# Kernel optimization log

Measured on AMD Instinct MI355X. Metric: run time of the kernel, lower is better.

## Reference

```python
import jax, jax.numpy as jnp
import numpy as np

NUM_FREQ = 10
HIDDEN = 256
ENC_DIM = 2 * 2 * NUM_FREQ  # input_dim * 2 * num_frequencies = 40
OUT_DIM = 3


def setup_inputs() -> dict:
    key = jax.random.key(0)
    ks = jax.random.split(key, 8)
    B, N = 4, 262144
    x = jax.random.uniform(ks[0], (B, N, 2), dtype=jnp.float32)
    # layer 0: enc_dim -> hidden
    W_in = jax.random.normal(ks[1], (ENC_DIM, HIDDEN), dtype=jnp.float32) * (1.0 / np.sqrt(ENC_DIM))
    b_in = jnp.zeros((HIDDEN,), dtype=jnp.float32)
    # layers 1..6: hidden -> hidden (6 of them)
    W_hid = jax.random.normal(ks[2], (6, HIDDEN, HIDDEN), dtype=jnp.float32) * (1.0 / np.sqrt(HIDDEN))
    b_hid = jnp.zeros((6, HIDDEN), dtype=jnp.float32)
    # layer 7: hidden -> out
    W_out = jax.random.normal(ks[3], (HIDDEN, OUT_DIM), dtype=jnp.float32) * (1.0 / np.sqrt(HIDDEN))
    b_out = jnp.zeros((OUT_DIM,), dtype=jnp.float32)
    return {"x": x, "W_in": W_in, "b_in": b_in, "W_hid": W_hid,
            "b_hid": b_hid, "W_out": W_out, "b_out": b_out}


def _pos_encode(x):
    # x: (B, N, 2) -> (B, N, 40). Matches torch: cat([sin, cos], -1) over freq axis then flatten.
    freq = 2.0 ** jnp.arange(NUM_FREQ, dtype=jnp.float32)  # (10,)
    xe = x[..., :, None] * freq  # (B, N, 2, 10)
    enc = jnp.concatenate([jnp.sin(xe), jnp.cos(xe)], axis=-1)  # (B, N, 2, 20)
    return enc.reshape(x.shape[0], x.shape[1], -1)  # (B, N, 40)


def reference(x, W_in, b_in, W_hid, b_hid, W_out, b_out):
    h = _pos_encode(x)
    h = jax.nn.relu(h @ W_in + b_in)
    for i in range(W_hid.shape[0]):  # 6 hidden layers, fixed small loop
        h = jax.nn.relu(h @ W_hid[i] + b_hid[i])
    out = jnp.tanh(h @ W_out + b_out) / 100.0
    return out
```

## Files before the change

kernel.cpp:

```cpp
#include <hip/hip_runtime.h>
#include <stdint.h>

#define THREADS 512
#define NBLOCKS 8192
#define BR      128

#define NG_STRIDE 204800
#define WS_WOUT   819200
#define WS_TOTAL  (WS_WOUT + 16384)

typedef short bf16x8 __attribute__((ext_vector_type(8)));
typedef float f32x16 __attribute__((ext_vector_type(16)));
typedef float f32x4v __attribute__((ext_vector_type(4)));

__device__ __forceinline__ unsigned short f2bf(float f) {
    union { float f; unsigned int u; } v; v.f = f;
    unsigned int u = v.u;
    u += 0x7fffu + ((u >> 16) & 1u);
    return (unsigned short)(u >> 16);
}
__device__ __forceinline__ unsigned int cvt_pk_bf16(float lo, float hi) {
    unsigned int d;
    asm("v_cvt_pk_bf16_f32 %0, %1, %2" : "=v"(d) : "v"(lo), "v"(hi));
    return d;
}

__global__ void prep_kernel(const float* __restrict__ W_in,
                            const float* __restrict__ W_hid,
                            const float* __restrict__ W_out,
                            unsigned char* __restrict__ ws) {
    int id = blockIdx.x * 256 + threadIdx.x;
    if (id < 16384) {
        int n = id & 255, k = id >> 8;
        int ng = n >> 6, ft = (n >> 5) & 1, ln = n & 31;
        int kk = k >> 4, hi = (k >> 3) & 1, e = k & 7;
        float v = (k < 40) ? W_in[k * 256 + n] : 0.f;
        *(unsigned short*)(ws + ng * NG_STRIDE + (kk * 2 + ft) * 1024
                           + (hi * 32 + ln) * 16 + e * 2) = f2bf(v);
    } else if (id < 16384 + 393216) {
        int e2 = id - 16384;
        int l = e2 >> 16, r = e2 & 65535;
        int k = r >> 8, n = r & 255;
        int c = k >> 6, kk = (k >> 4) & 3, hi = (k >> 3) & 1, e = k & 7;
        int ng = n >> 6, ft = (n >> 5) & 1, ln = n & 31;
        float v = W_hid[l * 65536 + k * 256 + n];
        *(unsigned short*)(ws + ng * NG_STRIDE + 8192 + l * 32768
                           + ((c * 4 + kk) * 2 + ft) * 1024
                           + (hi * 32 + ln) * 16 + e * 2) = f2bf(v);
    } else if (id < 16384 + 393216 + 8192) {
        int e3 = id - 16384 - 393216;
        int n = e3 >> 8, k = e3 & 255;
        int kk = k >> 4, hi = (k >> 3) & 1, e = k & 7;
        float v = (n < 3) ? W_out[k * 3 + n] : 0.f;
        *(unsigned short*)(ws + WS_WOUT + kk * 1024
                           + (hi * 32 + n) * 16 + e * 2) = f2bf(v);
    }
}

template <int NC>
__device__ __forceinline__ void layer_pass(const unsigned char* __restrict__ wl,
                                           const float* __restrict__ bp,
                                           unsigned char* actL, f32x16 (&acc)[2][2],
                                           int nblk, int rblk, int l31,
                                           int hi, int hi16, int swz) {
    #pragma unroll
    for (int tn = 0; tn < 2; ++tn) {
        #pragma unroll
        for (int g4 = 0; g4 < 4; ++g4) {
            f32x4v bv = *(const f32x4v*)(bp + nblk + tn * 32 + g4 * 8 + hi * 4);
            #pragma unroll
            for (int j = 0; j < 4; ++j) {
                acc[tn][0][g4 * 4 + j] = bv[j];
                acc[tn][1][g4 * 4 + j] = bv[j];
            }
        }
    }
    const unsigned char* br0 = actL + (rblk      + l31) * 512;
    const unsigned char* br1 = actL + (rblk + 32 + l31) * 512;
    int io[4];
    #pragma unroll
    for (int kk = 0; kk < 4; ++kk) io[kk] = (kk * 32 + hi16) ^ swz;

    __builtin_amdgcn_s_setprio(1);
    #pragma unroll
    for (int c = 0; c < NC; ++c) {
        #pragma unroll
        for (int kk = 0; kk < 4; ++kk) {
            const unsigned char* fp = wl + (c * 4 + kk) * 2048;
            bf16x8 a0 = *(const bf16x8*)(fp);
            bf16x8 a1 = *(const bf16x8*)(fp + 1024);
            bf16x8 b0 = *(const bf16x8*)(br0 + c * 128 + io[kk]);
            bf16x8 b1 = *(const bf16x8*)(br1 + c * 128 + io[kk]);
            acc[0][0] = __builtin_amdgcn_mfma_f32_32x32x16_bf16(a0, b0, acc[0][0], 0, 0, 0);
            acc[1][0] = __builtin_amdgcn_mfma_f32_32x32x16_bf16(a1, b0, acc[1][0], 0, 0, 0);
            acc[0][1] = __builtin_amdgcn_mfma_f32_32x32x16_bf16(a0, b1, acc[0][1], 0, 0, 0);
            acc[1][1] = __builtin_amdgcn_mfma_f32_32x32x16_bf16(a1, b1, acc[1][1], 0, 0, 0);
        }
    }
    __builtin_amdgcn_s_setprio(0);

    __syncthreads();
    #pragma unroll
    for (int tr = 0; tr < 2; ++tr) {
        unsigned char* rowp = actL + (rblk + tr * 32 + l31) * 512;
        #pragma unroll
        for (int tn = 0; tn < 2; ++tn) {
            #pragma unroll
            for (int g4 = 0; g4 < 4; ++g4) {
                float v0 = fmaxf(acc[tn][tr][g4 * 4 + 0], 0.f);
                float v1 = fmaxf(acc[tn][tr][g4 * 4 + 1], 0.f);
                float v2 = fmaxf(acc[tn][tr][g4 * 4 + 2], 0.f);
                float v3 = fmaxf(acc[tn][tr][g4 * 4 + 3], 0.f);
                int n0b = (nblk + tn * 32 + g4 * 8 + hi * 4) * 2;
                uint2 u; u.x = cvt_pk_bf16(v0, v1); u.y = cvt_pk_bf16(v2, v3);
                *(uint2*)(rowp + (n0b ^ swz)) = u;
            }
        }
    }
    __syncthreads();
}

__global__ __launch_bounds__(THREADS, 4)
void nerf_main(const float* __restrict__ x,
               const float* __restrict__ b_in,
               const float* __restrict__ b_hid,
               const float* __restrict__ b_out,
               const unsigned char* __restrict__ ws,
               float* __restrict__ out) {
    __shared__ __align__(16) unsigned char actL[65536];

    const int tid  = threadIdx.x;
    const int lane = tid & 63;
    const int wv   = tid >> 6;
    const int l31  = lane & 31;
    const int hi   = lane >> 5;
    const int hi16 = hi << 4;
    const int swz  = (l31 & 7) << 4;
    const int ng   = wv & 3,  nblk = ng * 64;
    const int rg   = wv >> 2, rblk = rg * 64;
    const long gr0 = (long)blockIdx.x * BR;

    {
        const int rr = tid >> 2, part = tid & 3;
        const int co = part >> 1, hf = part & 1;
        float xv = x[(gr0 + rr) * 2 + co];
        unsigned char* rowp = actL + rr * 512;
        const int rsw = (rr & 7) << 4;
        const int kb = co * 20 + hf * 10;
        float vv[10];
        #pragma unroll
        for (int f = 0; f < 10; ++f) {
            float ang = xv * (float)(1 << f);
            vv[f] = hf ? __cosf(ang) : __sinf(ang);
        }
        #pragma unroll
        for (int p = 0; p < 5; ++p) {
            unsigned int u = cvt_pk_bf16(vv[2 * p], vv[2 * p + 1]);
            int byte = (kb + 2 * p) * 2;
            *(unsigned int*)(rowp + (byte ^ rsw)) = u;
        }
        int z = 80 + part * 12;
        *(unsigned int*)(rowp + ((z    ) ^ rsw)) = 0u;
        *(unsigned int*)(rowp + ((z + 4) ^ rsw)) = 0u;
        *(unsigned int*)(rowp + ((z + 8) ^ rsw)) = 0u;
    }
    __syncthreads();

    f32x16 acc[2][2];
    const unsigned char* wstream = ws + ng * NG_STRIDE + lane * 16;

    layer_pass<1>(wstream, b_in, actL, acc, nblk, rblk, l31, hi, hi16, swz);
    wstream += 8192;

    #pragma unroll 1
    for (int l = 0; l < 6; ++l) {
        layer_pass<4>(wstream, b_hid + l * 256,
                      actL, acc, nblk, rblk, l31, hi, hi16, swz);
        wstream += 32768;
    }

    if (wv < 4) {
        f32x16 c0, c1;
        #pragma unroll
        for (int j = 0; j < 16; ++j) { c0[j] = 0.f; c1[j] = 0.f; }
        const unsigned char* wo   = ws + WS_WOUT + lane * 16;
        const unsigned char* arow = actL + (wv * 32 + l31) * 512;
        #pragma unroll
        for (int kk = 0; kk < 16; ++kk) {
            bf16x8 a = *(const bf16x8*)(wo + kk * 1024);
            bf16x8 b = *(const bf16x8*)(arow + (((kk * 32 + hi16)) ^ swz));
            if (kk & 1) c1 = __builtin_amdgcn_mfma_f32_32x32x16_bf16(a, b, c1, 0, 0, 0);
            else        c0 = __builtin_amdgcn_mfma_f32_32x32x16_bf16(a, b, c0, 0, 0, 0);
        }
        if (hi == 0) {
            long row = gr0 + wv * 32 + l31;
            float* op = out + row * 3;
            #pragma unroll
            for (int j = 0; j < 3; ++j)
                op[j] = tanhf(c0[j] + c1[j] + b_out[j]) * 0.01f;
        }
    }
}

extern "C" void kernel_launch(void* const* d_in, const int* in_sizes, int n_in,
                              void* d_out, int out_size, void* d_ws, size_t ws_size,
                              hipStream_t stream) {
    (void)in_sizes; (void)n_in; (void)out_size;
    const float* x     = (const float*)d_in[0];
    const float* W_in  = (const float*)d_in[1];
    const float* b_in  = (const float*)d_in[2];
    const float* W_hid = (const float*)d_in[3];
    const float* b_hid = (const float*)d_in[4];
    const float* W_out = (const float*)d_in[5];
    const float* b_out = (const float*)d_in[6];
    unsigned char* ws  = (unsigned char*)d_ws;
    float* out = (float*)d_out;

    if (ws_size < (size_t)WS_TOTAL) return;

    prep_kernel<<<1632, 256, 0, stream>>>(W_in, W_hid, W_out, ws);
    nerf_main<<<NBLOCKS, THREADS, 0, stream>>>(x, b_in, b_hid, b_out, ws, out);
}
```

Baseline: 818.5 us.

## Halve block threads so each wave computes all 128 rows

The block drops from 8 waves to 4. Each wave now covers all 128 rows of its 64-column slice, with a 2x4 MFMA accumulator tile instead of 2x2. Every weight fragment loaded from global memory is reused across twice as many rows, halving weight traffic per output, and the final output layer now runs on all four waves. In exchange, accumulator registers per thread double (launch bounds drop to 2 blocks per EU), which reduces occupancy and latency hiding.

After: 731.2 us. -10.7%, faster.

```diff
diff --git a/kernel.cpp b/kernel.cpp
--- a/kernel.cpp
+++ b/kernel.cpp
@@ -1,7 +1,7 @@
 #include <hip/hip_runtime.h>
 #include <stdint.h>
 
-#define THREADS 512
+#define THREADS 256
 #define NBLOCKS 8192
 #define BR      128
 
@@ -60,8 +60,8 @@
 template <int NC>
 __device__ __forceinline__ void layer_pass(const unsigned char* __restrict__ wl,
                                            const float* __restrict__ bp,
-                                           unsigned char* actL, f32x16 (&acc)[2][2],
-                                           int nblk, int rblk, int l31,
+                                           unsigned char* actL, f32x16 (&acc)[2][4],
+                                           int nblk, int l31,
                                            int hi, int hi16, int swz) {
     #pragma unroll
     for (int tn = 0; tn < 2; ++tn) {
@@ -69,14 +69,14 @@
         for (int g4 = 0; g4 < 4; ++g4) {
             f32x4v bv = *(const f32x4v*)(bp + nblk + tn * 32 + g4 * 8 + hi * 4);
             #pragma unroll
-            for (int j = 0; j < 4; ++j) {
-                acc[tn][0][g4 * 4 + j] = bv[j];
-                acc[tn][1][g4 * 4 + j] = bv[j];
+            for (int tr = 0; tr < 4; ++tr) {
+                #pragma unroll
+                for (int j = 0; j < 4; ++j)
+                    acc[tn][tr][g4 * 4 + j] = bv[j];
             }
         }
     }
-    const unsigned char* br0 = actL + (rblk      + l31) * 512;
-    const unsigned char* br1 = actL + (rblk + 32 + l31) * 512;
+
     int io[4];
     #pragma unroll
     for (int kk = 0; kk < 4; ++kk) io[kk] = (kk * 32 + hi16) ^ swz;
@@ -89,20 +89,27 @@
             const unsigned char* fp = wl + (c * 4 + kk) * 2048;
             bf16x8 a0 = *(const bf16x8*)(fp);
             bf16x8 a1 = *(const bf16x8*)(fp + 1024);
-            bf16x8 b0 = *(const bf16x8*)(br0 + c * 128 + io[kk]);
-            bf16x8 b1 = *(const bf16x8*)(br1 + c * 128 + io[kk]);
+            const int bo = c * 128 + io[kk];
+            bf16x8 b0 = *(const bf16x8*)(actL + (      l31) * 512 + bo);
+            bf16x8 b1 = *(const bf16x8*)(actL + (32  + l31) * 512 + bo);
+            bf16x8 b2 = *(const bf16x8*)(actL + (64  + l31) * 512 + bo);
+            bf16x8 b3 = *(const bf16x8*)(actL + (96  + l31) * 512 + bo);
             acc[0][0] = __builtin_amdgcn_mfma_f32_32x32x16_bf16(a0, b0, acc[0][0], 0, 0, 0);
             acc[1][0] = __builtin_amdgcn_mfma_f32_32x32x16_bf16(a1, b0, acc[1][0], 0, 0, 0);
             acc[0][1] = __builtin_amdgcn_mfma_f32_32x32x16_bf16(a0, b1, acc[0][1], 0, 0, 0);
             acc[1][1] = __builtin_amdgcn_mfma_f32_32x32x16_bf16(a1, b1, acc[1][1], 0, 0, 0);
+            acc[0][2] = __builtin_amdgcn_mfma_f32_32x32x16_bf16(a0, b2, acc[0][2], 0, 0, 0);
+            acc[1][2] = __builtin_amdgcn_mfma_f32_32x32x16_bf16(a1, b2, acc[1][2], 0, 0, 0);
+            acc[0][3] = __builtin_amdgcn_mfma_f32_32x32x16_bf16(a0, b3, acc[0][3], 0, 0, 0);
+            acc[1][3] = __builtin_amdgcn_mfma_f32_32x32x16_bf16(a1, b3, acc[1][3], 0, 0, 0);
         }
     }
     __builtin_amdgcn_s_setprio(0);
 
     __syncthreads();
     #pragma unroll
-    for (int tr = 0; tr < 2; ++tr) {
-        unsigned char* rowp = actL + (rblk + tr * 32 + l31) * 512;
+    for (int tr = 0; tr < 4; ++tr) {
+        unsigned char* rowp = actL + (tr * 32 + l31) * 512;
         #pragma unroll
         for (int tn = 0; tn < 2; ++tn) {
             #pragma unroll
@@ -120,7 +127,7 @@
     __syncthreads();
 }
 
-__global__ __launch_bounds__(THREADS, 4)
+__global__ __launch_bounds__(THREADS, 2)
 void nerf_main(const float* __restrict__ x,
                const float* __restrict__ b_in,
                const float* __restrict__ b_hid,
@@ -136,12 +143,13 @@
     const int hi   = lane >> 5;
     const int hi16 = hi << 4;
     const int swz  = (l31 & 7) << 4;
-    const int ng   = wv & 3,  nblk = ng * 64;
-    const int rg   = wv >> 2, rblk = rg * 64;
+    const int nblk = wv * 64;
     const long gr0 = (long)blockIdx.x * BR;
 
-    {
-        const int rr = tid >> 2, part = tid & 3;
+    #pragma unroll
+    for (int pass = 0; pass < 2; ++pass) {
+        const int rr = (tid >> 2) + pass * 64;
+        const int part = tid & 3;
         const int co = part >> 1, hf = part & 1;
         float xv = x[(gr0 + rr) * 2 + co];
         unsigned char* rowp = actL + rr * 512;
@@ -166,20 +174,20 @@
     }
     __syncthreads();
 
-    f32x16 acc[2][2];
-    const unsigned char* wstream = ws + ng * NG_STRIDE + lane * 16;
-
-    layer_pass<1>(wstream, b_in, actL, acc, nblk, rblk, l31, hi, hi16, swz);
+    f32x16 acc[2][4];
+    const unsigned char* wstream = ws + wv * NG_STRIDE + lane * 16;
+
+    layer_pass<1>(wstream, b_in, actL, acc, nblk, l31, hi, hi16, swz);
     wstream += 8192;
 
     #pragma unroll 1
     for (int l = 0; l < 6; ++l) {
         layer_pass<4>(wstream, b_hid + l * 256,
-                      actL, acc, nblk, rblk, l31, hi, hi16, swz);
+                      actL, acc, nblk, l31, hi, hi16, swz);
         wstream += 32768;
     }
 
-    if (wv < 4) {
+    {
         f32x16 c0, c1;
         #pragma unroll
         for (int j = 0; j < 16; ++j) { c0[j] = 0.f; c1[j] = 0.f; }
```
